# Kernel optimization log

Hardware: AMD Instinct MI355X
Metric: run time of the kernel (lower is better)

The kernel has to match this reference:

```python
import jax, jax.numpy as jnp
import numpy as np

B, S, D, H, DH = 2, 2048, 1024, 16, 64
ATTN_SCALE = float(np.sqrt(DH))  # use_attn_scale=True -> sqrt(d_head)
IGNORE = -100000.0


def setup_inputs() -> dict:
    key = jax.random.key(0)
    ks = jax.random.split(key, 8)
    init = 0.02
    return {
        "residual": jax.random.normal(ks[0], (B, S, D), dtype=jnp.float32),
        "x": jax.random.normal(ks[1], (B, S, D), dtype=jnp.float32),
        "W_Q": jax.random.normal(ks[2], (H, D, DH), dtype=jnp.float32) * init,
        "W_K": jax.random.normal(ks[3], (H, D, DH), dtype=jnp.float32) * init,
        "W_V": jax.random.normal(ks[4], (H, D, DH), dtype=jnp.float32) * init,
        "W_O": jax.random.normal(ks[5], (H, DH, D), dtype=jnp.float32) * init,
        "b_Q": jnp.zeros((H, DH), dtype=jnp.float32),
        "b_K": jnp.zeros((H, DH), dtype=jnp.float32),
        "b_V": jnp.zeros((H, DH), dtype=jnp.float32),
        "b_O": jnp.zeros((D,), dtype=jnp.float32),
    }


def reference(residual, x, W_Q, W_K, W_V, W_O, b_Q, b_K, b_V, b_O):
    # QKV projections: [b,s,d] x [h,d,e] -> [b,s,h,e]
    q = jnp.einsum("bsd,hde->bshe", x, W_Q) + b_Q
    k = jnp.einsum("bsd,hde->bshe", x, W_K) + b_K
    v = jnp.einsum("bsd,hde->bshe", x, W_V) + b_V
    # Scores: [b,h,q,k]
    attn_scores = jnp.einsum("bqhe,bkhe->bhqk", q, k) / ATTN_SCALE
    causal = jnp.tril(jnp.ones((S, S), dtype=bool))
    attn_scores = jnp.where(causal, attn_scores, IGNORE)
    pattern = jax.nn.softmax(attn_scores, axis=-1)
    # Weighted values: [b,q,h,e]
    z = jnp.einsum("bkhe,bhqk->bqhe", v, pattern)
    out = jnp.einsum("bqhe,hed->bqd", z, W_O) + b_O
    return (residual, out)
```

## Files before the change

kernel.cpp:

```cpp
#include <hip/hip_runtime.h>
#include <hip/hip_bf16.h>

#define BB 2
#define SS 2048
#define DD 1024
#define HH 16
#define DHD 64

typedef __attribute__((ext_vector_type(8))) short short8;
typedef __attribute__((ext_vector_type(4))) float floatx4;
typedef __attribute__((ext_vector_type(16))) float floatx16;
typedef __attribute__((ext_vector_type(4))) unsigned short ushortx4;

static __device__ __forceinline__ unsigned short f2bf(float f) {
    union { __hip_bfloat16 h; unsigned short u; } cv;
    cv.h = __float2bfloat16(f);
    return cv.u;
}

typedef __attribute__((address_space(1))) const unsigned int* gas_t;
typedef __attribute__((address_space(3))) unsigned int* las_t;
static __device__ __forceinline__ void g2l16(const void* g, void* l) {
    __builtin_amdgcn_global_load_lds((gas_t)g, (las_t)l, 16, 0, 0);
}

#define SW(row, c8) ((c8) ^ ((row) & 7))

static __device__ __forceinline__ unsigned cvt_pk_bf16(float lo, float hi) {
    unsigned r;
    asm("v_cvt_pk_bf16_f32 %0, %1, %2" : "=v"(r) : "v"(lo), "v"(hi));
    return r;
}
static __device__ __forceinline__ void pl32_swap(unsigned &a, unsigned &b) {
    asm("v_permlane32_swap_b32 %0, %1" : "+v"(a), "+v"(b));
}

__global__ __launch_bounds__(256) void prep(const float4* __restrict__ residual4,
        float4* __restrict__ out4,
        const float* __restrict__ x, unsigned short* __restrict__ xb,
        const float* __restrict__ WQ, const float* __restrict__ WK,
        const float* __restrict__ WV, unsigned short* __restrict__ Wt,
        const float* __restrict__ WO, unsigned short* __restrict__ WtO) {
    __shared__ float tile[64][65];
    const int bid = blockIdx.x;
    const int t = threadIdx.x;

    if (bid < 1024) {
        size_t base = (size_t)bid * 1024 + t;
#pragma unroll
        for (int j = 0; j < 4; j++) out4[base + j * 256] = residual4[base + j * 256];
    } else if (bid < 3072) {
        size_t i = ((size_t)(bid - 1024) * 256 + t) * 8;
        const float* src = x + i;
        short8 o;
#pragma unroll
        for (int j = 0; j < 8; j++) o[j] = (short)f2bf(src[j]);
        *(short8*)(xb + i) = o;
    } else if (bid < 3840) {
        int u = bid - 3072;
        const int d0 = (u & 15) * 64;
        const int h  = (u >> 4) & 15;
        const int which = u >> 8;
        const float* W = (which == 0) ? WQ : (which == 1) ? WK : WV;
        const float* src = W + (size_t)h * DD * DHD;
#pragma unroll
        for (int i = 0; i < 16; i++) {
            int idx = i * 256 + t;
            int r = idx >> 6, c = idx & 63;
            tile[r][c] = src[(size_t)(d0 + r) * DHD + c];
        }
        __syncthreads();
        unsigned short* dst = Wt + ((size_t)which * 1024 + h * 64) * DD;
#pragma unroll
        for (int i = 0; i < 16; i++) {
            int idx = i * 256 + t;
            int e = idx >> 6, d = idx & 63;
            dst[(size_t)e * DD + d0 + d] = f2bf(tile[d][e]);
        }
    } else {
        int u = bid - 3840;
        const int k0 = (u & 15) * 64;
        const int n0 = (u >> 4) * 64;
#pragma unroll
        for (int i = 0; i < 16; i++) {
            int idx = i * 256 + t;
            int r = idx >> 6, c = idx & 63;
            tile[r][c] = WO[(size_t)(k0 + r) * DD + n0 + c];
        }
        __syncthreads();
#pragma unroll
        for (int i = 0; i < 16; i++) {
            int idx = i * 256 + t;
            int n = idx >> 6, kk = idx & 63;
            WtO[(size_t)(n0 + n) * DD + k0 + kk] = f2bf(tile[kk][n]);
        }
    }
}

__global__ __launch_bounds__(256) void qkv_mfma(const unsigned short* __restrict__ xb,
        const unsigned short* __restrict__ Wt,
        const float* __restrict__ bQ, const float* __restrict__ bK,
        const float* __restrict__ bV,
        unsigned short* __restrict__ oq, unsigned short* __restrict__ ok,
        unsigned short* __restrict__ ov) {
    __shared__ unsigned short smem[128 * 132];
    unsigned short* As = smem;
    unsigned short* Bs = smem + 128 * 64;

    const int m0 = blockIdx.x * 128;
    const int y  = blockIdx.y;
    const int which = y >> 3;
    const int h0 = (y & 7) * 2;
    const float* bias = (which == 0) ? bQ : (which == 1) ? bK : bV;
    unsigned short* ob = (which == 0) ? oq : (which == 1) ? ok : ov;
    const float scale = (which == 0) ? 0.125f : 1.0f;
    const unsigned short* Wb = Wt + (size_t)y * 128 * DD;

    const int t = threadIdx.x;
    const int lane = t & 63, w = t >> 6;
    const int l15 = lane & 15, quad = lane >> 4;

    floatx4 acc[2][8];
#pragma unroll
    for (int mt = 0; mt < 2; mt++)
#pragma unroll
        for (int nt = 0; nt < 8; nt++) acc[mt][nt] = floatx4{0.f, 0.f, 0.f, 0.f};

    for (int k0 = 0; k0 < DD; k0 += 64) {
#pragma unroll
        for (int i = 0; i < 4; i++) {
            int c = i * 256 + t;
            int row = c >> 3, c8 = c & 7;
            g2l16(xb + (size_t)(m0 + row) * DD + k0 + SW(row, c8) * 8, As + c * 8);
        }
#pragma unroll
        for (int i = 0; i < 4; i++) {
            int c = i * 256 + t;
            int row = c >> 3, c8 = c & 7;
            g2l16(Wb + (size_t)row * DD + k0 + SW(row, c8) * 8, Bs + c * 8);
        }
        __syncthreads();
#pragma unroll
        for (int ks = 0; ks < 2; ks++) {
            short8 af[2], bf[8];
#pragma unroll
            for (int mt = 0; mt < 2; mt++)
                af[mt] = *(const short8*)(As + (w * 32 + mt * 16 + l15) * 64 +
                                          SW(l15, ks * 4 + quad) * 8);
#pragma unroll
            for (int nt = 0; nt < 8; nt++)
                bf[nt] = *(const short8*)(Bs + (nt * 16 + l15) * 64 +
                                          SW(l15, ks * 4 + quad) * 8);
#pragma unroll
            for (int mt = 0; mt < 2; mt++)
#pragma unroll
                for (int nt = 0; nt < 8; nt++)
                    acc[mt][nt] = __builtin_amdgcn_mfma_f32_16x16x32_bf16(
                        af[mt], bf[nt], acc[mt][nt], 0, 0, 0);
        }
        __syncthreads();
    }

    if (which == 2) {
        unsigned short* T = smem;
#pragma unroll
        for (int mt = 0; mt < 2; mt++)
#pragma unroll
            for (int r = 0; r < 4; r++) {
                int mloc = w * 32 + mt * 16 + quad * 4 + r;
#pragma unroll
                for (int nt = 0; nt < 8; nt++) {
                    int n = nt * 16 + l15;
                    int h = h0 + (n >> 6), e = n & 63;
                    T[n * 132 + mloc] = f2bf(acc[mt][nt][r] + bias[h * DHD + e]);
                }
            }
        __syncthreads();
        const int b = m0 >> 11;
        const int s_base = m0 & (SS - 1);
#pragma unroll
        for (int i = 0; i < 8; i++) {
            int u = i * 256 + t;
            int row = u >> 4, c8 = u & 15;
            int h = h0 + (row >> 6), e = row & 63;
            *(short8*)(ov + (((size_t)b * HH + h) * DHD + e) * SS + s_base + c8 * 8) =
                *(const short8*)(T + row * 132 + c8 * 8);
        }
    } else {
#pragma unroll
        for (int mt = 0; mt < 2; mt++) {
#pragma unroll
            for (int r = 0; r < 4; r++) {
                int m = m0 + w * 32 + mt * 16 + quad * 4 + r;
                int b = m >> 11, s = m & (SS - 1);
#pragma unroll
                for (int nt = 0; nt < 8; nt++) {
                    int h = h0 + (nt >> 2);
                    int e = (nt & 3) * 16 + l15;
                    float v = (acc[mt][nt][r] + bias[h * DHD + e]) * scale;
                    ob[(((size_t)b * HH + h) * SS + s) * DHD + e] = f2bf(v);
                }
            }
        }
    }
}

#define KVT 128
__global__ __launch_bounds__(512, 4) void attn(const unsigned short* __restrict__ q,
        const unsigned short* __restrict__ k, const unsigned short* __restrict__ vt,
        unsigned short* __restrict__ z) {
    __shared__ unsigned short smem[32768];

    const int i0 = blockIdx.x;
    int bh, qt;
    if (i0 < 256) { bh = i0 & 31;         qt = 15 - (i0 >> 5); }
    else          { bh = (i0 - 256) & 31; qt = (i0 - 256) >> 5; }
    const int b  = bh >> 4, h = bh & (HH - 1);
    const int q0 = qt * 128;

    const int t = threadIdx.x;
    const int lane = t & 63;
    const int w = t >> 6;
    const int qsub = w & 3;
    const int grp  = w >> 2;
    const int l31 = lane & 31;
    const int hi = lane >> 5;

    const unsigned short* qb  = q  + (size_t)bh * SS * DHD;
    const unsigned short* kb  = k  + (size_t)bh * SS * DHD;
    const unsigned short* vtb = vt + (size_t)bh * DHD * SS;

    const int qrow = q0 + qsub * 32 + l31;
    const int fmin = q0 + qsub * 32;

    short8 qf[4];
#pragma unroll
    for (int c = 0; c < 4; c++)
        qf[c] = *(const short8*)(qb + (size_t)qrow * DHD + c * 16 + hi * 8);

    floatx16 o_acc[2];
#pragma unroll
    for (int eh = 0; eh < 2; eh++)
#pragma unroll
        for (int i = 0; i < 16; i++) o_acc[eh][i] = 0.f;
    float lsum = 0.f;

    int koff[4], voff[4];
#pragma unroll
    for (int c = 0; c < 4; c++)
        koff[c] = (grp * 64 + l31) * 64 + (((2 * c + hi) ^ (l31 & 7)) * 8);
#pragma unroll
    for (int ch = 0; ch < 4; ch++)
        voff[ch] = l31 * 128 + (((grp * 8 + ch * 2 + hi) ^ (l31 & 15)) * 8);

    const int nit = qt + 1;

#pragma unroll
    for (int i = 0; i < 2; i++) {
        int u = i * 512 + t, r = u >> 3, c8 = u & 7;
        g2l16(kb + (size_t)r * DHD + (c8 ^ (r & 7)) * 8, smem + u * 8);
    }
#pragma unroll
    for (int i = 0; i < 2; i++) {
        int u = i * 512 + t, e = u >> 4, c16 = u & 15;
        g2l16(vtb + (size_t)e * SS + (c16 ^ (e & 15)) * 8, smem + 16384 + u * 8);
    }

    for (int it = 0; it < nit; it++) {
        const int cur = it & 1;
        __syncthreads();
        if (it + 1 < nit) {
            const int nxt = cur ^ 1;
            const int kbase = (it + 1) * KVT;
#pragma unroll
            for (int i = 0; i < 2; i++) {
                int u = i * 512 + t, r = u >> 3, c8 = u & 7;
                g2l16(kb + (size_t)(kbase + r) * DHD + (c8 ^ (r & 7)) * 8,
                      smem + nxt * 8192 + u * 8);
            }
#pragma unroll
            for (int i = 0; i < 2; i++) {
                int u = i * 512 + t, e = u >> 4, c16 = u & 15;
                g2l16(vtb + (size_t)e * SS + kbase + (c16 ^ (e & 15)) * 8,
                      smem + 16384 + nxt * 8192 + u * 8);
            }
        }

        const unsigned short* Kc = smem + cur * 8192;
        const unsigned short* Vc = smem + 16384 + cur * 8192;
        const int tb = it * KVT + grp * 64;

#pragma unroll
        for (int st = 0; st < 2; st++) {
            const int kvb = tb + st * 32;
            if (kvb > fmin + 31) continue;

            floatx16 sacc;
#pragma unroll
            for (int i = 0; i < 16; i++) sacc[i] = 0.f;
#pragma unroll
            for (int c = 0; c < 4; c++) {
                short8 af = *(const short8*)(Kc + st * 2048 + koff[c]);
                sacc = __builtin_amdgcn_mfma_f32_32x32x16_bf16(af, qf[c], sacc,
                                                               0, 0, 0);
            }

            unsigned wv[8];
            if (kvb + 31 <= fmin) {
#pragma unroll
                for (int r2 = 0; r2 < 8; r2++) {
                    float p0 = __expf(sacc[2 * r2]);
                    float p1 = __expf(sacc[2 * r2 + 1]);
                    lsum += p0 + p1;
                    wv[r2] = cvt_pk_bf16(p0, p1);
                }
            } else {
#pragma unroll
                for (int r2 = 0; r2 < 8; r2++) {
                    const int ra = 2 * r2, rb = 2 * r2 + 1;
                    const int kva = kvb + (ra & 3) + 8 * (ra >> 2) + 4 * hi;
                    const int kvc = kvb + (rb & 3) + 8 * (rb >> 2) + 4 * hi;
                    float p0 = (kva <= qrow) ? __expf(sacc[ra]) : 0.f;
                    float p1 = (kvc <= qrow) ? __expf(sacc[rb]) : 0.f;
                    lsum += p0 + p1;
                    wv[r2] = cvt_pk_bf16(p0, p1);
                }
            }
            pl32_swap(wv[0], wv[2]);
            pl32_swap(wv[1], wv[3]);
            pl32_swap(wv[4], wv[6]);
            pl32_swap(wv[5], wv[7]);
            union { unsigned u[4]; short8 s; } u0, u1;
            u0.u[0] = wv[0]; u0.u[1] = wv[1]; u0.u[2] = wv[2]; u0.u[3] = wv[3];
            u1.u[0] = wv[4]; u1.u[1] = wv[5]; u1.u[2] = wv[6]; u1.u[3] = wv[7];
            const short8 pb0 = u0.s, pb1 = u1.s;

#pragma unroll
            for (int eh = 0; eh < 2; eh++) {
                short8 vf0 = *(const short8*)(Vc + eh * 4096 + voff[2 * st]);
                o_acc[eh] = __builtin_amdgcn_mfma_f32_32x32x16_bf16(
                    vf0, pb0, o_acc[eh], 0, 0, 0);
                short8 vf1 = *(const short8*)(Vc + eh * 4096 + voff[2 * st + 1]);
                o_acc[eh] = __builtin_amdgcn_mfma_f32_32x32x16_bf16(
                    vf1, pb1, o_acc[eh], 0, 0, 0);
            }
        }
    }

    lsum += __shfl_xor(lsum, 32);
    float* cm = (float*)smem;
    float* slot = cm + (qsub * 64 + lane) * 33;
    __syncthreads();
    if (grp == 1) {
#pragma unroll
        for (int eh = 0; eh < 2; eh++)
#pragma unroll
            for (int i = 0; i < 16; i++) slot[eh * 16 + i] = o_acc[eh][i];
        slot[32] = lsum;
    }
    __syncthreads();
    if (grp == 0) {
#pragma unroll
        for (int eh = 0; eh < 2; eh++)
#pragma unroll
            for (int i = 0; i < 16; i++) o_acc[eh][i] += slot[eh * 16 + i];
        const float inv = 1.f / (lsum + slot[32]);
        unsigned short* zr = z + ((size_t)b * SS + qrow) * (HH * DHD) + h * DHD;
#pragma unroll
        for (int eh = 0; eh < 2; eh++)
#pragma unroll
            for (int g = 0; g < 4; g++) {
                ushortx4 o;
#pragma unroll
                for (int m = 0; m < 4; m++) o[m] = f2bf(o_acc[eh][g * 4 + m] * inv);
                *(ushortx4*)(zr + eh * 32 + g * 8 + 4 * hi) = o;
            }
    }
}

__global__ __launch_bounds__(256) void out_mfma(const unsigned short* __restrict__ zb,
        const unsigned short* __restrict__ WtO, const float* __restrict__ bo,
        float* __restrict__ out) {
    __shared__ unsigned short As[64 * 64];
    __shared__ unsigned short Bs[128 * 64];

    const int m0 = blockIdx.x * 64;
    const int n0 = blockIdx.y * 128;
    const int t = threadIdx.x;
    const int lane = t & 63, w = t >> 6;
    const int l15 = lane & 15, quad = lane >> 4;

    floatx4 acc[8];
#pragma unroll
    for (int nt = 0; nt < 8; nt++) acc[nt] = floatx4{0.f, 0.f, 0.f, 0.f};

    for (int k0 = 0; k0 < DD; k0 += 64) {
#pragma unroll
        for (int i = 0; i < 2; i++) {
            int c = i * 256 + t;
            int row = c >> 3, c8 = c & 7;
            g2l16(zb + (size_t)(m0 + row) * DD + k0 + SW(row, c8) * 8, As + c * 8);
        }
#pragma unroll
        for (int i = 0; i < 4; i++) {
            int c = i * 256 + t;
            int row = c >> 3, c8 = c & 7;
            g2l16(WtO + (size_t)(n0 + row) * DD + k0 + SW(row, c8) * 8, Bs + c * 8);
        }
        __syncthreads();
#pragma unroll
        for (int ks = 0; ks < 2; ks++) {
            short8 af = *(const short8*)(As + (w * 16 + l15) * 64 +
                                         SW(l15, ks * 4 + quad) * 8);
#pragma unroll
            for (int nt = 0; nt < 8; nt++) {
                short8 bf = *(const short8*)(Bs + (nt * 16 + l15) * 64 +
                                             SW(l15, ks * 4 + quad) * 8);
                acc[nt] = __builtin_amdgcn_mfma_f32_16x16x32_bf16(
                    af, bf, acc[nt], 0, 0, 0);
            }
        }
        __syncthreads();
    }
#pragma unroll
    for (int r = 0; r < 4; r++) {
        int m = m0 + w * 16 + quad * 4 + r;
#pragma unroll
        for (int nt = 0; nt < 8; nt++) {
            int n = n0 + nt * 16 + l15;
            out[(size_t)m * DD + n] = acc[nt][r] + bo[n];
        }
    }
}

extern "C" void kernel_launch(void* const* d_in, const int* in_sizes, int n_in,
                              void* d_out, int out_size, void* d_ws, size_t ws_size,
                              hipStream_t stream) {
    const float* residual = (const float*)d_in[0];
    const float* x   = (const float*)d_in[1];
    const float* W_Q = (const float*)d_in[2];
    const float* W_K = (const float*)d_in[3];
    const float* W_V = (const float*)d_in[4];
    const float* W_O = (const float*)d_in[5];
    const float* b_Q = (const float*)d_in[6];
    const float* b_K = (const float*)d_in[7];
    const float* b_V = (const float*)d_in[8];
    const float* b_O = (const float*)d_in[9];
    float* out = (float*)d_out;

    const size_t NE = (size_t)BB * SS * HH * DHD;
    unsigned short* xb  = (unsigned short*)d_ws;
    unsigned short* Wt  = xb + (size_t)4096 * 1024;
    unsigned short* WtO = Wt + (size_t)3072 * 1024;
    unsigned short* qb  = WtO + (size_t)1024 * 1024;
    unsigned short* kb  = qb + NE;
    unsigned short* vb  = kb + NE;
    unsigned short* zb  = vb + NE;

    prep<<<4096, 256, 0, stream>>>((const float4*)residual, (float4*)out,
                                   x, xb, W_Q, W_K, W_V, Wt, W_O, WtO);

    qkv_mfma<<<dim3(32, 24), 256, 0, stream>>>(xb, Wt, b_Q, b_K, b_V, qb, kb, vb);

    attn<<<512, 512, 0, stream>>>(qb, kb, vb, zb);

    out_mfma<<<dim3(64, 8), 256, 0, stream>>>(
        zb, WtO, b_O, out + (size_t)BB * SS * DD);
}
```

Before: 196.0 us.

## Double-buffer LDS tiles in QKV and output GEMMs, shrink output N-tile

Both projection GEMMs now keep two LDS buffers. The next K-slice is prefetched with global_load_lds while the MFMAs run on the current slice, and each k-step uses one barrier instead of two. The output GEMM also halves its N tile from 128 to 64 and doubles the grid, giving more blocks to spread across CUs. In exchange the QKV kernel uses 64KB of LDS, which may cut occupancy, and the smaller output tile reloads the A operand more often.

```diff
diff --git a/kernel.cpp b/kernel.cpp
--- a/kernel.cpp
+++ b/kernel.cpp
@@ -103,9 +103,7 @@
         const float* __restrict__ bV,
         unsigned short* __restrict__ oq, unsigned short* __restrict__ ok,
         unsigned short* __restrict__ ov) {
-    __shared__ unsigned short smem[128 * 132];
-    unsigned short* As = smem;
-    unsigned short* Bs = smem + 128 * 64;
+    __shared__ unsigned short smem[32768];
 
     const int m0 = blockIdx.x * 128;
     const int y  = blockIdx.y;
@@ -126,20 +124,31 @@
 #pragma unroll
         for (int nt = 0; nt < 8; nt++) acc[mt][nt] = floatx4{0.f, 0.f, 0.f, 0.f};
 
+#pragma unroll
+    for (int i = 0; i < 4; i++) {
+        int c = i * 256 + t;
+        int row = c >> 3, c8 = c & 7;
+        g2l16(xb + (size_t)(m0 + row) * DD + SW(row, c8) * 8, smem + c * 8);
+        g2l16(Wb + (size_t)row * DD + SW(row, c8) * 8, smem + 16384 + c * 8);
+    }
+
+    int buf = 0;
     for (int k0 = 0; k0 < DD; k0 += 64) {
-#pragma unroll
-        for (int i = 0; i < 4; i++) {
-            int c = i * 256 + t;
-            int row = c >> 3, c8 = c & 7;
-            g2l16(xb + (size_t)(m0 + row) * DD + k0 + SW(row, c8) * 8, As + c * 8);
-        }
-#pragma unroll
-        for (int i = 0; i < 4; i++) {
-            int c = i * 256 + t;
-            int row = c >> 3, c8 = c & 7;
-            g2l16(Wb + (size_t)row * DD + k0 + SW(row, c8) * 8, Bs + c * 8);
-        }
-        __syncthreads();
+        __syncthreads();
+        if (k0 + 64 < DD) {
+            const int nb = buf ^ 1;
+#pragma unroll
+            for (int i = 0; i < 4; i++) {
+                int c = i * 256 + t;
+                int row = c >> 3, c8 = c & 7;
+                g2l16(xb + (size_t)(m0 + row) * DD + k0 + 64 + SW(row, c8) * 8,
+                      smem + nb * 8192 + c * 8);
+                g2l16(Wb + (size_t)row * DD + k0 + 64 + SW(row, c8) * 8,
+                      smem + 16384 + nb * 8192 + c * 8);
+            }
+        }
+        const unsigned short* As = smem + buf * 8192;
+        const unsigned short* Bs = smem + 16384 + buf * 8192;
 #pragma unroll
         for (int ks = 0; ks < 2; ks++) {
             short8 af[2], bf[8];
@@ -158,8 +167,9 @@
                     acc[mt][nt] = __builtin_amdgcn_mfma_f32_16x16x32_bf16(
                         af[mt], bf[nt], acc[mt][nt], 0, 0, 0);
         }
-        __syncthreads();
-    }
+        buf ^= 1;
+    }
+    __syncthreads();
 
     if (which == 2) {
         unsigned short* T = smem;
@@ -381,52 +391,62 @@
 __global__ __launch_bounds__(256) void out_mfma(const unsigned short* __restrict__ zb,
         const unsigned short* __restrict__ WtO, const float* __restrict__ bo,
         float* __restrict__ out) {
-    __shared__ unsigned short As[64 * 64];
-    __shared__ unsigned short Bs[128 * 64];
+    __shared__ unsigned short smem[16384];
 
     const int m0 = blockIdx.x * 64;
-    const int n0 = blockIdx.y * 128;
+    const int n0 = blockIdx.y * 64;
     const int t = threadIdx.x;
     const int lane = t & 63, w = t >> 6;
     const int l15 = lane & 15, quad = lane >> 4;
 
-    floatx4 acc[8];
-#pragma unroll
-    for (int nt = 0; nt < 8; nt++) acc[nt] = floatx4{0.f, 0.f, 0.f, 0.f};
-
+    floatx4 acc[4];
+#pragma unroll
+    for (int nt = 0; nt < 4; nt++) acc[nt] = floatx4{0.f, 0.f, 0.f, 0.f};
+
+#pragma unroll
+    for (int i = 0; i < 2; i++) {
+        int c = i * 256 + t;
+        int row = c >> 3, c8 = c & 7;
+        g2l16(zb + (size_t)(m0 + row) * DD + SW(row, c8) * 8, smem + c * 8);
+        g2l16(WtO + (size_t)(n0 + row) * DD + SW(row, c8) * 8, smem + 8192 + c * 8);
+    }
+
+    int buf = 0;
     for (int k0 = 0; k0 < DD; k0 += 64) {
-#pragma unroll
-        for (int i = 0; i < 2; i++) {
-            int c = i * 256 + t;
-            int row = c >> 3, c8 = c & 7;
-            g2l16(zb + (size_t)(m0 + row) * DD + k0 + SW(row, c8) * 8, As + c * 8);
-        }
-#pragma unroll
-        for (int i = 0; i < 4; i++) {
-            int c = i * 256 + t;
-            int row = c >> 3, c8 = c & 7;
-            g2l16(WtO + (size_t)(n0 + row) * DD + k0 + SW(row, c8) * 8, Bs + c * 8);
-        }
-        __syncthreads();
+        __syncthreads();
+        if (k0 + 64 < DD) {
+            const int nb = buf ^ 1;
+#pragma unroll
+            for (int i = 0; i < 2; i++) {
+                int c = i * 256 + t;
+                int row = c >> 3, c8 = c & 7;
+                g2l16(zb + (size_t)(m0 + row) * DD + k0 + 64 + SW(row, c8) * 8,
+                      smem + nb * 4096 + c * 8);
+                g2l16(WtO + (size_t)(n0 + row) * DD + k0 + 64 + SW(row, c8) * 8,
+                      smem + 8192 + nb * 4096 + c * 8);
+            }
+        }
+        const unsigned short* As = smem + buf * 4096;
+        const unsigned short* Bs = smem + 8192 + buf * 4096;
 #pragma unroll
         for (int ks = 0; ks < 2; ks++) {
             short8 af = *(const short8*)(As + (w * 16 + l15) * 64 +
                                          SW(l15, ks * 4 + quad) * 8);
 #pragma unroll
-            for (int nt = 0; nt < 8; nt++) {
+            for (int nt = 0; nt < 4; nt++) {
                 short8 bf = *(const short8*)(Bs + (nt * 16 + l15) * 64 +
                                              SW(l15, ks * 4 + quad) * 8);
                 acc[nt] = __builtin_amdgcn_mfma_f32_16x16x32_bf16(
                     af, bf, acc[nt], 0, 0, 0);
             }
         }
-        __syncthreads();
+        buf ^= 1;
     }
 #pragma unroll
     for (int r = 0; r < 4; r++) {
         int m = m0 + w * 16 + quad * 4 + r;
 #pragma unroll
-        for (int nt = 0; nt < 8; nt++) {
+        for (int nt = 0; nt < 4; nt++) {
             int n = n0 + nt * 16 + l15;
             out[(size_t)m * DD + n] = acc[nt][r] + bo[n];
         }
@@ -464,6 +484,6 @@
 
     attn<<<512, 512, 0, stream>>>(qb, kb, vb, zb);
 
-    out_mfma<<<dim3(64, 8), 256, 0, stream>>>(
+    out_mfma<<<dim3(64, 16), 256, 0, stream>>>(
         zb, WtO, b_O, out + (size_t)BB * SS * DD);
 }
```

New measurement: 180.4 us. 7.9% less time.
